# Performance work log

Hardware: AMD Instinct MI355X
Metric: run time of the kernel (lower is better)

## Reference

```python
import jax, jax.numpy as jnp
import numpy as np

B, L, H, E, V = 64, 2048, 256, 256, 50257  # batch, max_length, hidden, embed, vocab


def setup_inputs() -> dict:
    key = jax.random.key(0)
    ks = jax.random.split(key, 16)
    s = 0.02
    return {
        "input_idx": jax.random.randint(ks[0], (B,), 0, V),
        "encoder_outputs": jax.random.normal(ks[1], (B, L, 2 * H), jnp.float32),
        "input_seq_idx": jax.random.randint(ks[2], (B, L), 0, V),
        "pre_state": jax.random.normal(ks[3], (B, H), jnp.float32),
        "pre_prob_c": jax.random.uniform(ks[4], (B, L), jnp.float32),
        "embed_table": jax.random.normal(ks[5], (V, E), jnp.float32) * s,
        "attn_W": jax.random.normal(ks[6], (2 * H, L), jnp.float32) * s,
        "attn_b": jnp.zeros((L,), jnp.float32),
        "gru_Wih": jax.random.normal(ks[7], (3 * H, E + 2 * H), jnp.float32) * s,
        "gru_Whh": jax.random.normal(ks[8], (3 * H, H), jnp.float32) * s,
        "gru_bih": jnp.zeros((3 * H,), jnp.float32),
        "gru_bhh": jnp.zeros((3 * H,), jnp.float32),
        "Wc_W": jax.random.normal(ks[9], (2 * H, H), jnp.float32) * s,
        "Wc_b": jnp.zeros((H,), jnp.float32),
        "Wo_W": jax.random.normal(ks[10], (H, V), jnp.float32) * s,
        "Wo_b": jnp.zeros((V,), jnp.float32),
    }


def reference(input_idx, encoder_outputs, input_seq_idx, pre_state, pre_prob_c,
              embed_table, attn_W, attn_b, gru_Wih, gru_Whh, gru_bih, gru_bhh,
              Wc_W, Wc_b, Wo_W, Wo_b):
    b, l, _ = encoder_outputs.shape
    h = pre_state.shape[1]
    v = Wo_b.shape[0]

    # --- attention over encoder positions ---
    emb = embed_table[input_idx]                                  # [B,E]
    attn_in = jnp.concatenate([emb, pre_state], axis=1)           # [B,2H]
    attn_weights = jax.nn.softmax(attn_in @ attn_W + attn_b, axis=1)  # [B,L]
    attn_applied = jnp.einsum('bl,bld->bd', attn_weights, encoder_outputs)  # [B,2H]

    # --- selective read (copy mechanism) ---
    match = (input_seq_idx == input_idx[:, None]).astype(encoder_outputs.dtype)  # [B,L]
    cnt = jnp.sum(match, axis=1, keepdims=True)
    match = match / jnp.maximum(cnt, 1.0)                         # normalize rows with >1 match
    select_weights = match * pre_prob_c                           # [B,L]
    select_applied = jnp.einsum('bl,bld->bd', select_weights, encoder_outputs)  # [B,2H]

    # --- GRU cell step (PyTorch GRU math) ---
    x = jnp.concatenate([emb, attn_applied + select_applied], axis=1)  # [B,E+2H]
    gi = x @ gru_Wih.T + gru_bih                                  # [B,3H]
    gh = pre_state @ gru_Whh.T + gru_bhh                          # [B,3H]
    i_r, i_z, i_n = jnp.split(gi, 3, axis=1)
    h_r, h_z, h_n = jnp.split(gh, 3, axis=1)
    r = jax.nn.sigmoid(i_r + h_r)
    z = jax.nn.sigmoid(i_z + h_z)
    n = jnp.tanh(i_n + r * h_n)
    state = (1.0 - z) * n + z * pre_state                         # [B,H]

    # --- generate + copy scores ---
    score_g = state @ Wo_W + Wo_b                                 # [B,V]
    score_c = jnp.einsum('blh,bh->bl',
                         jnp.tanh(encoder_outputs @ Wc_W + Wc_b), state)  # [B,L]
    prob = jax.nn.softmax(jnp.concatenate([score_g, score_c], axis=1), axis=1)  # [B,V+L]
    prob_g = prob[:, :v]
    prob_c = prob[:, v:]

    # --- scatter-add copy probs into extended vocab buffer ---
    rows = jnp.arange(b)[:, None]
    out = jnp.zeros((b, v + l), prob.dtype)
    out = out.at[rows, input_seq_idx].add(prob_c)
    out = out.at[:, :v].add(prob_g)
    return out, state, prob_c
```

## Files before the change

### kernel.cpp

```cpp
#include <hip/hip_runtime.h>

#define B_   64
#define L_   2048
#define H_   256
#define E_   256
#define V_   50257
#define TWOH 512
#define VL   52305

typedef short bf16x8 __attribute__((ext_vector_type(8)));
typedef float f32x4  __attribute__((ext_vector_type(4)));

__device__ inline unsigned short f2bf(float f){
  unsigned u = __float_as_uint(f);
  unsigned r = (u + 0x7fffu + ((u >> 16) & 1u)) >> 16;
  return (unsigned short)r;
}
__device__ inline float fast_tanh(float x){
  x = fminf(15.f, fmaxf(-15.f, x));
  float e = __expf(2.f * x);
  return (e - 1.f) / (e + 1.f);
}
__device__ inline float fast_sigmoid(float x){
  return 1.f / (1.f + __expf(-x));
}

__global__ __launch_bounds__(256) void k_prep(const float* __restrict__ Wc,
                                              unsigned short* __restrict__ WcT){
  int i = blockIdx.x * 256 + threadIdx.x;
  int n = i >> 9, k = i & 511;
  WcT[i] = f2bf(Wc[(size_t)k * 256 + n]);
}

__global__ __launch_bounds__(256) void k_setup(const int* __restrict__ idx, const int* __restrict__ seq,
    const float* __restrict__ embed, const float* __restrict__ pre_state,
    float* __restrict__ attn_in, float* __restrict__ applied, float* __restrict__ cnt){
  int b = blockIdx.x, t = threadIdx.x;
  int id = idx[b];
  attn_in[b * 512 + t]       = embed[(size_t)id * 256 + t];
  attn_in[b * 512 + 256 + t] = pre_state[b * 256 + t];
  applied[b * 512 + t] = 0.f;
  applied[b * 512 + 256 + t] = 0.f;
  int c = 0;
  for (int l = t; l < 2048; l += 256) c += (seq[b * 2048 + l] == id) ? 1 : 0;
  __shared__ int red[256];
  red[t] = c; __syncthreads();
  for (int o = 128; o; o >>= 1){ if (t < o) red[t] += red[t + o]; __syncthreads(); }
  if (t == 0) cnt[b] = (float)red[0];
}

__global__ __launch_bounds__(256) void k_logits(const float* __restrict__ attn_in,
    const float* __restrict__ attn_W, const float* __restrict__ attn_b, float* __restrict__ logits){
  int lt = blockIdx.x, b = blockIdx.y, t = threadIdx.x;
  int l = lt * 256 + t;
  __shared__ float ai[512];
  ai[t] = attn_in[b * 512 + t];
  ai[256 + t] = attn_in[b * 512 + 256 + t];
  __syncthreads();
  float acc = attn_b[l];
  for (int k4 = 0; k4 < 128; ++k4){
    const float4 a = *(const float4*)&ai[k4 * 4];
    acc += a.x * attn_W[(size_t)(k4 * 4 + 0) * 2048 + l]
         + a.y * attn_W[(size_t)(k4 * 4 + 1) * 2048 + l]
         + a.z * attn_W[(size_t)(k4 * 4 + 2) * 2048 + l]
         + a.w * attn_W[(size_t)(k4 * 4 + 3) * 2048 + l];
  }
  logits[b * 2048 + l] = acc;
}

__global__ __launch_bounds__(256) void k_weights(const float* __restrict__ logits,
    const int* __restrict__ seq, const int* __restrict__ idx, const float* __restrict__ ppc,
    const float* __restrict__ cnt, float* __restrict__ w){
  int b = blockIdx.x, t = threadIdx.x;
  float v[8];
  float m = -3e38f;
#pragma unroll
  for (int i = 0; i < 8; ++i){ v[i] = logits[b * 2048 + i * 256 + t]; m = fmaxf(m, v[i]); }
  __shared__ float red[256];
  red[t] = m; __syncthreads();
  for (int o = 128; o; o >>= 1){ if (t < o) red[t] = fmaxf(red[t], red[t + o]); __syncthreads(); }
  m = red[0]; __syncthreads();
  float s = 0.f;
#pragma unroll
  for (int i = 0; i < 8; ++i){ v[i] = __expf(v[i] - m); s += v[i]; }
  red[t] = s; __syncthreads();
  for (int o = 128; o; o >>= 1){ if (t < o) red[t] += red[t + o]; __syncthreads(); }
  float invZ = 1.f / red[0];
  int id = idx[b];
  float invc = 1.f / fmaxf(cnt[b], 1.f);
#pragma unroll
  for (int i = 0; i < 8; ++i){
    int l = i * 256 + t;
    float sw = (seq[b * 2048 + l] == id) ? ppc[b * 2048 + l] * invc : 0.f;
    w[b * 2048 + l] = v[i] * invZ + sw;
  }
}

__global__ __launch_bounds__(256) void k_applied(const float* __restrict__ enc,
    const float* __restrict__ w, float* __restrict__ applied){
  int lc = blockIdx.x, b = blockIdx.y, t = threadIdx.x;
  __shared__ float sw[256];
  sw[t] = w[b * 2048 + lc * 256 + t];
  __syncthreads();
  float ax = 0.f, ay = 0.f;
  for (int l = 0; l < 256; ++l){
    const float2 v = *(const float2*)(enc + ((size_t)b * 2048 + lc * 256 + l) * 512 + 2 * t);
    float wl = sw[l];
    ax += wl * v.x; ay += wl * v.y;
  }
  atomicAdd(&applied[b * 512 + 2 * t],     ax);
  atomicAdd(&applied[b * 512 + 2 * t + 1], ay);
}

__global__ __launch_bounds__(256) void k_gi(const float* __restrict__ attn_in,
    const float* __restrict__ applied, const float* __restrict__ Wih, float* __restrict__ gi){
  int wave = threadIdx.x >> 6, lane = threadIdx.x & 63;
  int b = blockIdx.y;
  int o0 = (blockIdx.x * 4 + wave) * 8;
  float a[12];
#pragma unroll
  for (int i = 0; i < 4; ++i)  a[i] = attn_in[b * 512 + lane + i * 64];
#pragma unroll
  for (int i = 0; i < 8; ++i)  a[4 + i] = applied[b * 512 + lane + i * 64];
  float acc[8];
#pragma unroll
  for (int r = 0; r < 8; ++r){
    const float* wrow = Wih + (size_t)(o0 + r) * 768;
    float s = 0.f;
#pragma unroll
    for (int i = 0; i < 12; ++i) s += a[i] * wrow[lane + i * 64];
    acc[r] = s;
  }
#pragma unroll
  for (int m = 1; m < 64; m <<= 1){
#pragma unroll
    for (int r = 0; r < 8; ++r) acc[r] += __shfl_xor(acc[r], m, 64);
  }
  if (lane == 0){
#pragma unroll
    for (int r = 0; r < 8; ++r) gi[(size_t)b * 768 + o0 + r] = acc[r];
  }
}

__global__ __launch_bounds__(256) void k_gh(const float* __restrict__ pre_state,
    const float* __restrict__ Whh, float* __restrict__ gh){
  int wave = threadIdx.x >> 6, lane = threadIdx.x & 63;
  int b = blockIdx.y;
  int o0 = (blockIdx.x * 4 + wave) * 8;
  float a[4];
#pragma unroll
  for (int i = 0; i < 4; ++i) a[i] = pre_state[b * 256 + lane + i * 64];
  float acc[8];
#pragma unroll
  for (int r = 0; r < 8; ++r){
    const float* wrow = Whh + (size_t)(o0 + r) * 256;
    float s = 0.f;
#pragma unroll
    for (int i = 0; i < 4; ++i) s += a[i] * wrow[lane + i * 64];
    acc[r] = s;
  }
#pragma unroll
  for (int m = 1; m < 64; m <<= 1){
#pragma unroll
    for (int r = 0; r < 8; ++r) acc[r] += __shfl_xor(acc[r], m, 64);
  }
  if (lane == 0){
#pragma unroll
    for (int r = 0; r < 8; ++r) gh[(size_t)b * 768 + o0 + r] = acc[r];
  }
}

__global__ __launch_bounds__(256) void k_gru2(const float* __restrict__ gi, const float* __restrict__ gh,
    const float* __restrict__ bih, const float* __restrict__ bhh, const float* __restrict__ pre_state,
    float* __restrict__ state, float* __restrict__ out_state){
  int b = blockIdx.x, t = threadIdx.x;
  float ir = gi[(size_t)b * 768 + t]       + bih[t];
  float iz = gi[(size_t)b * 768 + 256 + t] + bih[256 + t];
  float in_= gi[(size_t)b * 768 + 512 + t] + bih[512 + t];
  float hr = gh[(size_t)b * 768 + t]       + bhh[t];
  float hz = gh[(size_t)b * 768 + 256 + t] + bhh[256 + t];
  float hn = gh[(size_t)b * 768 + 512 + t] + bhh[512 + t];
  float r = fast_sigmoid(ir + hr);
  float z = fast_sigmoid(iz + hz);
  float n = fast_tanh(in_ + r * hn);
  float ps = pre_state[b * 256 + t];
  float st = (1.f - z) * n + z * ps;
  state[b * 256 + t] = st;
  out_state[b * 256 + t] = st;
}

__global__ __launch_bounds__(256) void k_scoreg(const float* __restrict__ Wo,
    const float* __restrict__ Wob, const float* __restrict__ state, float* __restrict__ out1){
  int v0 = blockIdx.x * 256;
  int tid = threadIdx.x;
  int wave = tid >> 6, lane = tid & 63;
  int lr = lane & 15, q = lane >> 4;
  __shared__ unsigned short sA[64 * 264];
  __shared__ unsigned short sB[256 * 40];
  for (int i = tid; i < 64 * 256; i += 256){
    int r = i >> 8, c = i & 255;
    sA[r * 264 + c] = f2bf(state[i]);
  }
  f32x4 zero = {0.f, 0.f, 0.f, 0.f};
  f32x4 acc[16];
#pragma unroll
  for (int i = 0; i < 16; ++i) acc[i] = zero;
  int v = v0 + tid;
  for (int kk = 0; kk < 8; ++kk){
    __syncthreads();
    for (int r = 0; r < 32; ++r){
      float val = (v < V_) ? Wo[(size_t)(kk * 32 + r) * V_ + v] : 0.f;
      sB[tid * 40 + r] = f2bf(val);
    }
    __syncthreads();
    bf16x8 af = *(const bf16x8*)&sA[(wave * 16 + lr) * 264 + kk * 32 + q * 8];
#pragma unroll
    for (int nf = 0; nf < 16; ++nf){
      bf16x8 bf = *(const bf16x8*)&sB[(nf * 16 + lr) * 40 + q * 8];
      acc[nf] = __builtin_amdgcn_mfma_f32_16x16x32_bf16(af, bf, acc[nf], 0, 0, 0);
    }
  }
#pragma unroll
  for (int nf = 0; nf < 16; ++nf){
    int vv = v0 + nf * 16 + lr;
    if (vv < V_){
      float wb = Wob[vv];
#pragma unroll
      for (int r = 0; r < 4; ++r){
        int bb = wave * 16 + q * 4 + r;
        out1[(size_t)bb * VL + vv] = acc[nf][r] + wb;
      }
    }
  }
}

__global__ __launch_bounds__(256) void k_scorec(const float* __restrict__ enc,
    const unsigned short* __restrict__ WcT, const float* __restrict__ Wcb,
    const float* __restrict__ state, float* __restrict__ score_c){
  int lt = blockIdx.x, b = blockIdx.y;
  int tid = threadIdx.x;
  int wave = tid >> 6, lane = tid & 63;
  int lr = lane & 15, q = lane >> 4;
  __shared__ unsigned short s_wc[256 * 40];
  __shared__ float s_state[256];
  __shared__ float s_bias[256];
  s_state[tid] = state[b * 256 + tid];
  s_bias[tid]  = Wcb[tid];
  f32x4 zero = {0.f, 0.f, 0.f, 0.f};
  f32x4 acc[16];
#pragma unroll
  for (int i = 0; i < 16; ++i) acc[i] = zero;
  const float* arow = enc + ((size_t)b * 2048 + lt * 64 + wave * 16 + lr) * 512;
  for (int kk = 0; kk < 16; ++kk){
    {
      const uint4* src = (const uint4*)(WcT + (size_t)tid * 512 + kk * 32);
      uint4* dst = (uint4*)&s_wc[tid * 40];
      dst[0] = src[0]; dst[1] = src[1]; dst[2] = src[2]; dst[3] = src[3];
    }
    __syncthreads();
    float4 a0 = *(const float4*)(arow + kk * 32 + q * 8);
    float4 a1 = *(const float4*)(arow + kk * 32 + q * 8 + 4);
    bf16x8 af;
    af[0] = f2bf(a0.x); af[1] = f2bf(a0.y); af[2] = f2bf(a0.z); af[3] = f2bf(a0.w);
    af[4] = f2bf(a1.x); af[5] = f2bf(a1.y); af[6] = f2bf(a1.z); af[7] = f2bf(a1.w);
#pragma unroll
    for (int nf = 0; nf < 16; ++nf){
      bf16x8 bf = *(const bf16x8*)&s_wc[(nf * 16 + lr) * 40 + q * 8];
      acc[nf] = __builtin_amdgcn_mfma_f32_16x16x32_bf16(af, bf, acc[nf], 0, 0, 0);
    }
    __syncthreads();
  }
  float part[4] = {0.f, 0.f, 0.f, 0.f};
#pragma unroll
  for (int nf = 0; nf < 16; ++nf){
    int col = nf * 16 + lr;
    float sv = s_state[col], bv = s_bias[col];
#pragma unroll
    for (int r = 0; r < 4; ++r){
      part[r] += fast_tanh(acc[nf][r] + bv) * sv;
    }
  }
#pragma unroll
  for (int m = 1; m <= 8; m <<= 1){
#pragma unroll
    for (int r = 0; r < 4; ++r) part[r] += __shfl_xor(part[r], m, 64);
  }
  if (lr == 0){
#pragma unroll
    for (int r = 0; r < 4; ++r)
      score_c[b * 2048 + lt * 64 + wave * 16 + q * 4 + r] = part[r];
  }
}

__global__ __launch_bounds__(256) void k_stats1(const float* __restrict__ out1,
    const float* __restrict__ score_c, float* __restrict__ part){
  int c = blockIdx.x, b = blockIdx.y, t = threadIdx.x;
  int i0 = c * 3328, i1 = i0 + 3328; if (i1 > VL) i1 = VL;
  float m = -3.0e38f, s = 0.f;
  for (int i = i0 + t; i < i1; i += 256){
    float v = (i < V_) ? out1[(size_t)b * VL + i] : score_c[b * 2048 + (i - V_)];
    if (v > m){ s = s * __expf(m - v) + 1.f; m = v; }
    else s += __expf(v - m);
  }
  __shared__ float ms[256], ss[256];
  ms[t] = m; ss[t] = s; __syncthreads();
  for (int o = 128; o; o >>= 1){
    if (t < o){
      float m2 = ms[t + o], s2 = ss[t + o];
      float mn = fmaxf(ms[t], m2);
      ss[t] = ss[t] * __expf(ms[t] - mn) + s2 * __expf(m2 - mn);
      ms[t] = mn;
    }
    __syncthreads();
  }
  if (t == 0){ part[(b * 16 + c) * 2] = ms[0]; part[(b * 16 + c) * 2 + 1] = ss[0]; }
}

__global__ __launch_bounds__(64) void k_stats2(const float* __restrict__ part, float* __restrict__ mz){
  int b = blockIdx.x, t = threadIdx.x;
  float m = -3.0e38f, s = 0.f;
  if (t < 16){ m = part[(b * 16 + t) * 2]; s = part[(b * 16 + t) * 2 + 1]; }
  for (int o = 1; o < 64; o <<= 1){
    float m2 = __shfl_xor(m, o, 64), s2 = __shfl_xor(s, o, 64);
    float mn = fmaxf(m, m2);
    s = s * __expf(m - mn) + s2 * __expf(m2 - mn);
    m = mn;
  }
  if (t == 0){ mz[2 * b] = m; mz[2 * b + 1] = s; }
}

__global__ __launch_bounds__(256) void k_probg(float* __restrict__ out1, const float* __restrict__ mz){
  int b = blockIdx.y;
  int i = blockIdx.x * 256 + threadIdx.x;
  if (i >= VL) return;
  float m = mz[2 * b], z = mz[2 * b + 1];
  float* row = out1 + (size_t)b * VL;
  row[i] = (i < V_) ? __expf(row[i] - m) / z : 0.f;
}

__global__ __launch_bounds__(256) void k_probc(const float* __restrict__ score_c,
    const float* __restrict__ mz, const int* __restrict__ seq,
    float* __restrict__ out1, float* __restrict__ out3){
  int b = blockIdx.y;
  int l = blockIdx.x * 256 + threadIdx.x;
  float m = mz[2 * b], z = mz[2 * b + 1];
  float p = __expf(score_c[b * 2048 + l] - m) / z;
  out3[b * 2048 + l] = p;
  atomicAdd(&out1[(size_t)b * VL + seq[b * 2048 + l]], p);
}

extern "C" void kernel_launch(void* const* d_in, const int* in_sizes, int n_in,
                              void* d_out, int out_size, void* d_ws, size_t ws_size,
                              hipStream_t stream) {
  const int*   idx      = (const int*)d_in[0];
  const float* enc      = (const float*)d_in[1];
  const int*   seq      = (const int*)d_in[2];
  const float* prestate = (const float*)d_in[3];
  const float* ppc      = (const float*)d_in[4];
  const float* embed    = (const float*)d_in[5];
  const float* attn_W   = (const float*)d_in[6];
  const float* attn_b   = (const float*)d_in[7];
  const float* Wih      = (const float*)d_in[8];
  const float* Whh      = (const float*)d_in[9];
  const float* bih      = (const float*)d_in[10];
  const float* bhh      = (const float*)d_in[11];
  const float* Wc       = (const float*)d_in[12];
  const float* Wcb      = (const float*)d_in[13];
  const float* Wo       = (const float*)d_in[14];
  const float* Wob      = (const float*)d_in[15];

  float* out1 = (float*)d_out;
  float* out2 = out1 + (size_t)B_ * VL;
  float* out3 = out2 + (size_t)B_ * H_;

  char* w8 = (char*)d_ws;
  unsigned short* WcT = (unsigned short*)(w8 + 0);
  float* attn_in = (float*)(w8 + 262144);
  float* logits  = (float*)(w8 + 393216);
  float* wgt     = (float*)(w8 + 917504);
  float* applied = (float*)(w8 + 1441792);
  float* state   = (float*)(w8 + 1572864);
  float* score_c = (float*)(w8 + 1638400);
  float* mz      = (float*)(w8 + 2162688);
  float* cnt     = (float*)(w8 + 2163200);
  float* gi      = (float*)(w8 + 2163456);
  float* gh      = (float*)(w8 + 2360064);
  float* part    = (float*)(w8 + 2556672);

  k_prep   <<<512, 256, 0, stream>>>(Wc, WcT);
  k_setup  <<<64, 256, 0, stream>>>(idx, seq, embed, prestate, attn_in, applied, cnt);
  k_logits <<<dim3(8, 64), 256, 0, stream>>>(attn_in, attn_W, attn_b, logits);
  k_weights<<<64, 256, 0, stream>>>(logits, seq, idx, ppc, cnt, wgt);
  k_applied<<<dim3(8, 64), 256, 0, stream>>>(enc, wgt, applied);
  k_gi     <<<dim3(24, 64), 256, 0, stream>>>(attn_in, applied, Wih, gi);
  k_gh     <<<dim3(24, 64), 256, 0, stream>>>(prestate, Whh, gh);
  k_gru2   <<<64, 256, 0, stream>>>(gi, gh, bih, bhh, prestate, state, out2);
  k_scoreg <<<197, 256, 0, stream>>>(Wo, Wob, state, out1);
  k_scorec <<<dim3(32, 64), 256, 0, stream>>>(enc, WcT, Wcb, state, score_c);
  k_stats1 <<<dim3(16, 64), 256, 0, stream>>>(out1, score_c, part);
  k_stats2 <<<64, 64, 0, stream>>>(part, mz);
  k_probg  <<<dim3(205, 64), 256, 0, stream>>>(out1, mz);
  k_probc  <<<dim3(8, 64), 256, 0, stream>>>(score_c, mz, seq, out1, out3);
}
```

Measured before the change: 735.3 us.

## Fuse encoder read for attention-apply and Wc projection; store tanh tile, retile score_g

Merges the weighted encoder sum with the Wc projection so the large encoder tensor is read once, before the GRU step. The bf16 tanh(enc@Wc+b) tile is written to workspace so the copy score becomes a cheap dot with state. Per-tile applied partials are reduced in a separate kernel instead of using global atomics. The diff also fuses the prep/setup and gi/gh launches and shrinks score_g tiles to 64 columns for more blocks. The cost is an extra 64 MB bf16 write and read of T, plus shared-memory atomics in the fused kernel.

```diff
diff --git a/kernel.cpp b/kernel.cpp
--- a/kernel.cpp
+++ b/kernel.cpp
@@ -16,6 +16,9 @@
   unsigned r = (u + 0x7fffu + ((u >> 16) & 1u)) >> 16;
   return (unsigned short)r;
 }
+__device__ inline float bf2f(unsigned short h){
+  return __uint_as_float(((unsigned)h) << 16);
+}
 __device__ inline float fast_tanh(float x){
   x = fminf(15.f, fmaxf(-15.f, x));
   float e = __expf(2.f * x);
@@ -25,22 +28,20 @@
   return 1.f / (1.f + __expf(-x));
 }
 
-__global__ __launch_bounds__(256) void k_prep(const float* __restrict__ Wc,
-                                              unsigned short* __restrict__ WcT){
-  int i = blockIdx.x * 256 + threadIdx.x;
-  int n = i >> 9, k = i & 511;
-  WcT[i] = f2bf(Wc[(size_t)k * 256 + n]);
-}
-
-__global__ __launch_bounds__(256) void k_setup(const int* __restrict__ idx, const int* __restrict__ seq,
+__global__ __launch_bounds__(256) void k_prep_setup(const float* __restrict__ Wc,
+    unsigned short* __restrict__ WcT, const int* __restrict__ idx, const int* __restrict__ seq,
     const float* __restrict__ embed, const float* __restrict__ pre_state,
-    float* __restrict__ attn_in, float* __restrict__ applied, float* __restrict__ cnt){
+    float* __restrict__ attn_in, float* __restrict__ cnt){
   int b = blockIdx.x, t = threadIdx.x;
+#pragma unroll
+  for (int j = 0; j < 8; ++j){
+    int i = b * 2048 + t * 8 + j;
+    int n = i >> 9, k = i & 511;
+    WcT[i] = f2bf(Wc[(size_t)k * 256 + n]);
+  }
   int id = idx[b];
   attn_in[b * 512 + t]       = embed[(size_t)id * 256 + t];
   attn_in[b * 512 + 256 + t] = pre_state[b * 256 + t];
-  applied[b * 512 + t] = 0.f;
-  applied[b * 512 + 256 + t] = 0.f;
   int c = 0;
   for (int l = t; l < 2048; l += 256) c += (seq[b * 2048 + l] == id) ? 1 : 0;
   __shared__ int red[256];
@@ -96,77 +97,136 @@
   }
 }
 
-__global__ __launch_bounds__(256) void k_applied(const float* __restrict__ enc,
-    const float* __restrict__ w, float* __restrict__ applied){
-  int lc = blockIdx.x, b = blockIdx.y, t = threadIdx.x;
-  __shared__ float sw[256];
-  sw[t] = w[b * 2048 + lc * 256 + t];
-  __syncthreads();
-  float ax = 0.f, ay = 0.f;
-  for (int l = 0; l < 256; ++l){
-    const float2 v = *(const float2*)(enc + ((size_t)b * 2048 + lc * 256 + l) * 512 + 2 * t);
-    float wl = sw[l];
-    ax += wl * v.x; ay += wl * v.y;
-  }
-  atomicAdd(&applied[b * 512 + 2 * t],     ax);
-  atomicAdd(&applied[b * 512 + 2 * t + 1], ay);
-}
-
-__global__ __launch_bounds__(256) void k_gi(const float* __restrict__ attn_in,
-    const float* __restrict__ applied, const float* __restrict__ Wih, float* __restrict__ gi){
+__global__ __launch_bounds__(256) void k_encT(const float* __restrict__ enc,
+    const unsigned short* __restrict__ WcT, const float* __restrict__ Wcb,
+    const float* __restrict__ w, unsigned short* __restrict__ T, float* __restrict__ part_applied){
+  int lt = blockIdx.x, b = blockIdx.y;
+  int tid = threadIdx.x;
+  int wave = tid >> 6, lane = tid & 63;
+  int lr = lane & 15, q = lane >> 4;
+  __shared__ unsigned short s_wc[256 * 40];
+  __shared__ float s_bias[256];
+  __shared__ float s_w[64];
+  __shared__ float s_app[512];
+  s_bias[tid] = Wcb[tid];
+  if (tid < 64) s_w[tid] = w[b * 2048 + lt * 64 + tid];
+  s_app[tid] = 0.f; s_app[256 + tid] = 0.f;
+  f32x4 zero = {0.f, 0.f, 0.f, 0.f};
+  f32x4 acc[16];
+#pragma unroll
+  for (int i = 0; i < 16; ++i) acc[i] = zero;
+  const float* arow = enc + ((size_t)b * 2048 + lt * 64 + wave * 16 + lr) * 512;
+  for (int kk = 0; kk < 16; ++kk){
+    {
+      const uint4* src = (const uint4*)(WcT + (size_t)tid * 512 + kk * 32);
+      uint4* dst = (uint4*)&s_wc[tid * 40];
+      dst[0] = src[0]; dst[1] = src[1]; dst[2] = src[2]; dst[3] = src[3];
+    }
+    __syncthreads();
+    float4 a0 = *(const float4*)(arow + kk * 32 + q * 8);
+    float4 a1 = *(const float4*)(arow + kk * 32 + q * 8 + 4);
+    float wrow = s_w[wave * 16 + lr];
+    float p[8] = {a0.x*wrow, a0.y*wrow, a0.z*wrow, a0.w*wrow,
+                  a1.x*wrow, a1.y*wrow, a1.z*wrow, a1.w*wrow};
+#pragma unroll
+    for (int m = 1; m <= 8; m <<= 1){
+#pragma unroll
+      for (int j = 0; j < 8; ++j) p[j] += __shfl_xor(p[j], m, 64);
+    }
+    if (lr == 0){
+#pragma unroll
+      for (int j = 0; j < 8; ++j) atomicAdd(&s_app[kk * 32 + q * 8 + j], p[j]);
+    }
+    bf16x8 af;
+    af[0] = f2bf(a0.x); af[1] = f2bf(a0.y); af[2] = f2bf(a0.z); af[3] = f2bf(a0.w);
+    af[4] = f2bf(a1.x); af[5] = f2bf(a1.y); af[6] = f2bf(a1.z); af[7] = f2bf(a1.w);
+#pragma unroll
+    for (int nf = 0; nf < 16; ++nf){
+      bf16x8 bf = *(const bf16x8*)&s_wc[(nf * 16 + lr) * 40 + q * 8];
+      acc[nf] = __builtin_amdgcn_mfma_f32_16x16x32_bf16(af, bf, acc[nf], 0, 0, 0);
+    }
+    __syncthreads();
+  }
+#pragma unroll
+  for (int nf = 0; nf < 16; ++nf){
+    int col = nf * 16 + lr;
+    float bv = s_bias[col];
+#pragma unroll
+    for (int r = 0; r < 4; ++r){
+      int row = lt * 64 + wave * 16 + q * 4 + r;
+      T[((size_t)b * 2048 + row) * 256 + col] = f2bf(fast_tanh(acc[nf][r] + bv));
+    }
+  }
+  part_applied[((size_t)b * 32 + lt) * 512 + tid]       = s_app[tid];
+  part_applied[((size_t)b * 32 + lt) * 512 + 256 + tid] = s_app[256 + tid];
+}
+
+__global__ __launch_bounds__(256) void k_appred(const float* __restrict__ part_applied,
+    float* __restrict__ applied){
+  int b = blockIdx.x, t = threadIdx.x;
+  float a0 = 0.f, a1 = 0.f;
+  for (int lt = 0; lt < 32; ++lt){
+    a0 += part_applied[((size_t)b * 32 + lt) * 512 + t];
+    a1 += part_applied[((size_t)b * 32 + lt) * 512 + 256 + t];
+  }
+  applied[b * 512 + t] = a0;
+  applied[b * 512 + 256 + t] = a1;
+}
+
+__global__ __launch_bounds__(256) void k_giGh(const float* __restrict__ attn_in,
+    const float* __restrict__ applied, const float* __restrict__ pre_state,
+    const float* __restrict__ Wih, const float* __restrict__ Whh,
+    float* __restrict__ gi, float* __restrict__ gh){
   int wave = threadIdx.x >> 6, lane = threadIdx.x & 63;
   int b = blockIdx.y;
-  int o0 = (blockIdx.x * 4 + wave) * 8;
-  float a[12];
-#pragma unroll
-  for (int i = 0; i < 4; ++i)  a[i] = attn_in[b * 512 + lane + i * 64];
-#pragma unroll
-  for (int i = 0; i < 8; ++i)  a[4 + i] = applied[b * 512 + lane + i * 64];
-  float acc[8];
-#pragma unroll
-  for (int r = 0; r < 8; ++r){
-    const float* wrow = Wih + (size_t)(o0 + r) * 768;
-    float s = 0.f;
-#pragma unroll
-    for (int i = 0; i < 12; ++i) s += a[i] * wrow[lane + i * 64];
-    acc[r] = s;
-  }
-#pragma unroll
-  for (int m = 1; m < 64; m <<= 1){
-#pragma unroll
-    for (int r = 0; r < 8; ++r) acc[r] += __shfl_xor(acc[r], m, 64);
-  }
-  if (lane == 0){
-#pragma unroll
-    for (int r = 0; r < 8; ++r) gi[(size_t)b * 768 + o0 + r] = acc[r];
-  }
-}
-
-__global__ __launch_bounds__(256) void k_gh(const float* __restrict__ pre_state,
-    const float* __restrict__ Whh, float* __restrict__ gh){
-  int wave = threadIdx.x >> 6, lane = threadIdx.x & 63;
-  int b = blockIdx.y;
-  int o0 = (blockIdx.x * 4 + wave) * 8;
-  float a[4];
-#pragma unroll
-  for (int i = 0; i < 4; ++i) a[i] = pre_state[b * 256 + lane + i * 64];
-  float acc[8];
-#pragma unroll
-  for (int r = 0; r < 8; ++r){
-    const float* wrow = Whh + (size_t)(o0 + r) * 256;
-    float s = 0.f;
-#pragma unroll
-    for (int i = 0; i < 4; ++i) s += a[i] * wrow[lane + i * 64];
-    acc[r] = s;
-  }
-#pragma unroll
-  for (int m = 1; m < 64; m <<= 1){
-#pragma unroll
-    for (int r = 0; r < 8; ++r) acc[r] += __shfl_xor(acc[r], m, 64);
-  }
-  if (lane == 0){
-#pragma unroll
-    for (int r = 0; r < 8; ++r) gh[(size_t)b * 768 + o0 + r] = acc[r];
+  if (blockIdx.x < 24){
+    int o0 = (blockIdx.x * 4 + wave) * 8;
+    float a[12];
+#pragma unroll
+    for (int i = 0; i < 4; ++i)  a[i] = attn_in[b * 512 + lane + i * 64];
+#pragma unroll
+    for (int i = 0; i < 8; ++i)  a[4 + i] = applied[b * 512 + lane + i * 64];
+    float acc[8];
+#pragma unroll
+    for (int r = 0; r < 8; ++r){
+      const float* wrow = Wih + (size_t)(o0 + r) * 768;
+      float s = 0.f;
+#pragma unroll
+      for (int i = 0; i < 12; ++i) s += a[i] * wrow[lane + i * 64];
+      acc[r] = s;
+    }
+#pragma unroll
+    for (int m = 1; m < 64; m <<= 1){
+#pragma unroll
+      for (int r = 0; r < 8; ++r) acc[r] += __shfl_xor(acc[r], m, 64);
+    }
+    if (lane == 0){
+#pragma unroll
+      for (int r = 0; r < 8; ++r) gi[(size_t)b * 768 + o0 + r] = acc[r];
+    }
+  } else {
+    int o0 = ((blockIdx.x - 24) * 4 + wave) * 8;
+    float a[4];
+#pragma unroll
+    for (int i = 0; i < 4; ++i) a[i] = pre_state[b * 256 + lane + i * 64];
+    float acc[8];
+#pragma unroll
+    for (int r = 0; r < 8; ++r){
+      const float* wrow = Whh + (size_t)(o0 + r) * 256;
+      float s = 0.f;
+#pragma unroll
+      for (int i = 0; i < 4; ++i) s += a[i] * wrow[lane + i * 64];
+      acc[r] = s;
+    }
+#pragma unroll
+    for (int m = 1; m < 64; m <<= 1){
+#pragma unroll
+      for (int r = 0; r < 8; ++r) acc[r] += __shfl_xor(acc[r], m, 64);
+    }
+    if (lane == 0){
+#pragma unroll
+      for (int r = 0; r < 8; ++r) gh[(size_t)b * 768 + o0 + r] = acc[r];
+    }
   }
 }
 
@@ -191,37 +251,39 @@
 
 __global__ __launch_bounds__(256) void k_scoreg(const float* __restrict__ Wo,
     const float* __restrict__ Wob, const float* __restrict__ state, float* __restrict__ out1){
-  int v0 = blockIdx.x * 256;
+  int v0 = blockIdx.x * 64;
   int tid = threadIdx.x;
   int wave = tid >> 6, lane = tid & 63;
   int lr = lane & 15, q = lane >> 4;
   __shared__ unsigned short sA[64 * 264];
-  __shared__ unsigned short sB[256 * 40];
+  __shared__ unsigned short sB[64 * 40];
   for (int i = tid; i < 64 * 256; i += 256){
     int r = i >> 8, c = i & 255;
     sA[r * 264 + c] = f2bf(state[i]);
   }
   f32x4 zero = {0.f, 0.f, 0.f, 0.f};
-  f32x4 acc[16];
-#pragma unroll
-  for (int i = 0; i < 16; ++i) acc[i] = zero;
-  int v = v0 + tid;
+  f32x4 acc[4];
+#pragma unroll
+  for (int i = 0; i < 4; ++i) acc[i] = zero;
+  int c = tid & 63, rg = tid >> 6;
+  int v = v0 + c;
   for (int kk = 0; kk < 8; ++kk){
     __syncthreads();
-    for (int r = 0; r < 32; ++r){
-      float val = (v < V_) ? Wo[(size_t)(kk * 32 + r) * V_ + v] : 0.f;
-      sB[tid * 40 + r] = f2bf(val);
+#pragma unroll
+    for (int j = 0; j < 8; ++j){
+      float val = (v < V_) ? Wo[(size_t)(kk * 32 + rg * 8 + j) * V_ + v] : 0.f;
+      sB[c * 40 + rg * 8 + j] = f2bf(val);
     }
     __syncthreads();
     bf16x8 af = *(const bf16x8*)&sA[(wave * 16 + lr) * 264 + kk * 32 + q * 8];
 #pragma unroll
-    for (int nf = 0; nf < 16; ++nf){
+    for (int nf = 0; nf < 4; ++nf){
       bf16x8 bf = *(const bf16x8*)&sB[(nf * 16 + lr) * 40 + q * 8];
       acc[nf] = __builtin_amdgcn_mfma_f32_16x16x32_bf16(af, bf, acc[nf], 0, 0, 0);
     }
   }
 #pragma unroll
-  for (int nf = 0; nf < 16; ++nf){
+  for (int nf = 0; nf < 4; ++nf){
     int vv = v0 + nf * 16 + lr;
     if (vv < V_){
       float wb = Wob[vv];
@@ -234,61 +296,28 @@
   }
 }
 
-__global__ __launch_bounds__(256) void k_scorec(const float* __restrict__ enc,
-    const unsigned short* __restrict__ WcT, const float* __restrict__ Wcb,
+__global__ __launch_bounds__(256) void k_scorec2(const unsigned short* __restrict__ T,
     const float* __restrict__ state, float* __restrict__ score_c){
   int lt = blockIdx.x, b = blockIdx.y;
   int tid = threadIdx.x;
-  int wave = tid >> 6, lane = tid & 63;
-  int lr = lane & 15, q = lane >> 4;
-  __shared__ unsigned short s_wc[256 * 40];
-  __shared__ float s_state[256];
-  __shared__ float s_bias[256];
-  s_state[tid] = state[b * 256 + tid];
-  s_bias[tid]  = Wcb[tid];
-  f32x4 zero = {0.f, 0.f, 0.f, 0.f};
-  f32x4 acc[16];
-#pragma unroll
-  for (int i = 0; i < 16; ++i) acc[i] = zero;
-  const float* arow = enc + ((size_t)b * 2048 + lt * 64 + wave * 16 + lr) * 512;
-  for (int kk = 0; kk < 16; ++kk){
-    {
-      const uint4* src = (const uint4*)(WcT + (size_t)tid * 512 + kk * 32);
-      uint4* dst = (uint4*)&s_wc[tid * 40];
-      dst[0] = src[0]; dst[1] = src[1]; dst[2] = src[2]; dst[3] = src[3];
-    }
-    __syncthreads();
-    float4 a0 = *(const float4*)(arow + kk * 32 + q * 8);
-    float4 a1 = *(const float4*)(arow + kk * 32 + q * 8 + 4);
-    bf16x8 af;
-    af[0] = f2bf(a0.x); af[1] = f2bf(a0.y); af[2] = f2bf(a0.z); af[3] = f2bf(a0.w);
-    af[4] = f2bf(a1.x); af[5] = f2bf(a1.y); af[6] = f2bf(a1.z); af[7] = f2bf(a1.w);
-#pragma unroll
-    for (int nf = 0; nf < 16; ++nf){
-      bf16x8 bf = *(const bf16x8*)&s_wc[(nf * 16 + lr) * 40 + q * 8];
-      acc[nf] = __builtin_amdgcn_mfma_f32_16x16x32_bf16(af, bf, acc[nf], 0, 0, 0);
-    }
-    __syncthreads();
-  }
-  float part[4] = {0.f, 0.f, 0.f, 0.f};
-#pragma unroll
-  for (int nf = 0; nf < 16; ++nf){
-    int col = nf * 16 + lr;
-    float sv = s_state[col], bv = s_bias[col];
-#pragma unroll
-    for (int r = 0; r < 4; ++r){
-      part[r] += fast_tanh(acc[nf][r] + bv) * sv;
-    }
-  }
-#pragma unroll
-  for (int m = 1; m <= 8; m <<= 1){
-#pragma unroll
-    for (int r = 0; r < 4; ++r) part[r] += __shfl_xor(part[r], m, 64);
-  }
-  if (lr == 0){
-#pragma unroll
-    for (int r = 0; r < 4; ++r)
-      score_c[b * 2048 + lt * 64 + wave * 16 + q * 4 + r] = part[r];
+  int g = tid >> 5, hl = tid & 31;
+  float st[8];
+  {
+    float4 s0 = *(const float4*)&state[b * 256 + hl * 8];
+    float4 s1 = *(const float4*)&state[b * 256 + hl * 8 + 4];
+    st[0]=s0.x; st[1]=s0.y; st[2]=s0.z; st[3]=s0.w;
+    st[4]=s1.x; st[5]=s1.y; st[6]=s1.z; st[7]=s1.w;
+  }
+#pragma unroll
+  for (int it = 0; it < 8; ++it){
+    int row = lt * 64 + g * 8 + it;
+    bf16x8 tv = *(const bf16x8*)&T[((size_t)b * 2048 + row) * 256 + hl * 8];
+    float acc = 0.f;
+#pragma unroll
+    for (int j = 0; j < 8; ++j) acc += bf2f((unsigned short)tv[j]) * st[j];
+#pragma unroll
+    for (int m = 1; m <= 16; m <<= 1) acc += __shfl_xor(acc, m, 64);
+    if (hl == 0) score_c[b * 2048 + row] = acc;
   }
 }
 
@@ -386,17 +415,18 @@
   float* gi      = (float*)(w8 + 2163456);
   float* gh      = (float*)(w8 + 2360064);
   float* part    = (float*)(w8 + 2556672);
-
-  k_prep   <<<512, 256, 0, stream>>>(Wc, WcT);
-  k_setup  <<<64, 256, 0, stream>>>(idx, seq, embed, prestate, attn_in, applied, cnt);
+  float* part_app= (float*)(w8 + 2564864);
+  unsigned short* T = (unsigned short*)(w8 + 8388608);
+
+  k_prep_setup<<<64, 256, 0, stream>>>(Wc, WcT, idx, seq, embed, prestate, attn_in, cnt);
   k_logits <<<dim3(8, 64), 256, 0, stream>>>(attn_in, attn_W, attn_b, logits);
   k_weights<<<64, 256, 0, stream>>>(logits, seq, idx, ppc, cnt, wgt);
-  k_applied<<<dim3(8, 64), 256, 0, stream>>>(enc, wgt, applied);
-  k_gi     <<<dim3(24, 64), 256, 0, stream>>>(attn_in, applied, Wih, gi);
-  k_gh     <<<dim3(24, 64), 256, 0, stream>>>(prestate, Whh, gh);
+  k_encT   <<<dim3(32, 64), 256, 0, stream>>>(enc, WcT, Wcb, wgt, T, part_app);
+  k_appred <<<64, 256, 0, stream>>>(part_app, applied);
+  k_giGh   <<<dim3(48, 64), 256, 0, stream>>>(attn_in, applied, prestate, Wih, Whh, gi, gh);
   k_gru2   <<<64, 256, 0, stream>>>(gi, gh, bih, bhh, prestate, state, out2);
-  k_scoreg <<<197, 256, 0, stream>>>(Wo, Wob, state, out1);
-  k_scorec <<<dim3(32, 64), 256, 0, stream>>>(enc, WcT, Wcb, state, score_c);
+  k_scoreg <<<786, 256, 0, stream>>>(Wo, Wob, state, out1);
+  k_scorec2<<<dim3(32, 64), 256, 0, stream>>>(T, state, score_c);
   k_stats1 <<<dim3(16, 64), 256, 0, stream>>>(out1, score_c, part);
   k_stats2 <<<64, 64, 0, stream>>>(part, mz);
   k_probg  <<<dim3(205, 64), 256, 0, stream>>>(out1, mz);
```

After: 641.5 us. 12.7% less time.
